# Kernel optimization log

Hardware: AMD Instinct MI355X
Metric: run time of the kernel (lower is better)

## Reference

```python
import jax, jax.numpy as jnp
import numpy as np

N = 100000   # nodes
E = 1600000  # edges
D = 128      # input feature dim
H = 128      # hidden dim
C = 10       # output classes
G = 64       # graphs in batch


def setup_inputs() -> dict:
    key = jax.random.key(0)
    ks = jax.random.split(key, 24)
    s = 0.02
    lin = lambda k, i, o: jax.random.normal(k, (i, o), jnp.float32) * s
    inp = {
        'x': jax.random.normal(ks[0], (N, D), jnp.float32),
        'edge_index': jax.random.randint(ks[1], (2, E), 0, N),
        'batch': jnp.sort(jax.random.randint(ks[2], (N,), 0, G)),
        # GIN conv 0: Linear(D,H)-ReLU-Linear(H,H)
        'w1_0': lin(ks[3], D, H), 'b1_0': jnp.zeros((H,), jnp.float32),
        'w2_0': lin(ks[4], H, H), 'b2_0': jnp.zeros((H,), jnp.float32),
        # GIN conv 1
        'w1_1': lin(ks[5], H, H), 'b1_1': jnp.zeros((H,), jnp.float32),
        'w2_1': lin(ks[6], H, H), 'b2_1': jnp.zeros((H,), jnp.float32),
        # GIN conv 2
        'w1_2': lin(ks[7], H, H), 'b1_2': jnp.zeros((H,), jnp.float32),
        'w2_2': lin(ks[8], H, H), 'b2_2': jnp.zeros((H,), jnp.float32),
        # LayerNorms (applied after layers 0 and 1)
        'ln_g0': jnp.ones((H,), jnp.float32), 'ln_b0': jnp.zeros((H,), jnp.float32),
        'ln_g1': jnp.ones((H,), jnp.float32), 'ln_b1': jnp.zeros((H,), jnp.float32),
        # post_mp: Linear(H,H) -> Dropout -> Linear(H,C)
        'pw1': lin(ks[9], H, H), 'pb1': jnp.zeros((H,), jnp.float32),
        'pw2': lin(ks[10], H, C), 'pb2': jnp.zeros((C,), jnp.float32),
    }
    return inp


def _gin_conv(x, src, dst, w1, b1, w2, b2):
    # GINConv with eps=0: MLP(x + sum_{j->i} x_j)
    agg = jax.ops.segment_sum(x[src], dst, num_segments=N)  # [N, d]
    h = x + agg
    h = jax.nn.relu(h @ w1 + b1) @ w2 + b2
    return h


def _layernorm(x, g, b, eps=1e-5):
    mu = jnp.mean(x, axis=-1, keepdims=True)
    var = jnp.var(x, axis=-1, keepdims=True)
    return (x - mu) * jax.lax.rsqrt(var + eps) * g + b


def reference(x, edge_index, batch,
              w1_0, b1_0, w2_0, b2_0,
              w1_1, b1_1, w2_1, b2_1,
              w1_2, b1_2, w2_2, b2_2,
              ln_g0, ln_b0, ln_g1, ln_b1,
              pw1, pb1, pw2, pb2):
    src, dst = edge_index[0], edge_index[1]
    convs = [(w1_0, b1_0, w2_0, b2_0), (w1_1, b1_1, w2_1, b2_1), (w1_2, b1_2, w2_2, b2_2)]
    lns = [(ln_g0, ln_b0), (ln_g1, ln_b1)]
    emb = x
    h = x
    for i in range(3):
        w1, b1, w2, b2 = convs[i]
        h = _gin_conv(h, src, dst, w1, b1, w2, b2)
        emb = h
        h = jax.nn.relu(h)
        # dropout p=0.25: identity in eval mode
        if i != 2:
            g, b = lns[i]
            h = _layernorm(h, g, b)
    # global mean pool over graphs
    sums = jax.ops.segment_sum(h, batch, num_segments=G)          # [G, H]
    cnts = jax.ops.segment_sum(jnp.ones((N,), h.dtype), batch, num_segments=G)
    pooled = sums / jnp.maximum(cnts, 1.0)[:, None]
    # post_mp (dropout identity in eval)
    z = pooled @ pw1 + pb1
    logits = z @ pw2 + pb2
    return emb, jax.nn.log_softmax(logits, axis=1)
```

## Files before the change

### kernel.cpp

```cpp
#include <hip/hip_runtime.h>

typedef __bf16 bf16_t;
typedef __bf16 bf16x8 __attribute__((ext_vector_type(8)));
typedef float floatx4 __attribute__((ext_vector_type(4)));

constexpr int N = 100000;
constexpr int E = 1600000;
constexpr int H = 128;
constexpr int G = 64;
constexpr int C = 10;
constexpr int NBLK = (N + 255) / 256;

constexpr int FPART = 8;
constexpr int FPART_SZ = (N + FPART - 1) / FPART;
constexpr int FCHUNK = 256;
constexpr int FCHUNK_E = E / FCHUNK;

__device__ inline float bflo(unsigned u) {
  return __builtin_bit_cast(float, u << 16);
}
__device__ inline float bfhi(unsigned u) {
  return __builtin_bit_cast(float, u & 0xffff0000u);
}
__device__ inline unsigned short f2b(float f) {
  return __builtin_bit_cast(unsigned short, (bf16_t)f);
}
__device__ inline unsigned pack2(float a, float b) {
  return (unsigned)f2b(a) | ((unsigned)f2b(b) << 16);
}

__global__ __launch_bounds__(256) void tobf_kernel(const float* __restrict__ x,
                                                   uint4* __restrict__ xb) {
  const int g = blockIdx.x * 256 + threadIdx.x;
  const float4 a = *(const float4*)(x + (size_t)g * 8);
  const float4 b = *(const float4*)(x + (size_t)g * 8 + 4);
  uint4 o;
  o.x = pack2(a.x, a.y);
  o.y = pack2(a.z, a.w);
  o.z = pack2(b.x, b.y);
  o.w = pack2(b.z, b.w);
  xb[g] = o;
}

__global__ __launch_bounds__(256) void hist_kernel(const int* __restrict__ dst,
                                                   int* __restrict__ deg) {
  const int e = blockIdx.x * 256 + threadIdx.x;
  if (e < E) atomicAdd(&deg[dst[e]], 1);
}

__global__ __launch_bounds__(256) void partial_kernel(
    const int* __restrict__ deg, int* __restrict__ partials) {
  __shared__ int sm[256];
  const int tid = threadIdx.x;
  const int i = blockIdx.x * 256 + tid;
  sm[tid] = (i < N) ? deg[i] : 0;
  __syncthreads();
  for (int off = 128; off > 0; off >>= 1) {
    if (tid < off) sm[tid] += sm[tid + off];
    __syncthreads();
  }
  if (tid == 0) partials[blockIdx.x] = sm[0];
}

__global__ __launch_bounds__(512) void scanp_kernel(
    const int* __restrict__ partials, int* __restrict__ blockbase) {
  __shared__ int p[512];
  const int t = threadIdx.x;
  p[t] = (t < NBLK) ? partials[t] : 0;
  __syncthreads();
  for (int off = 1; off < 512; off <<= 1) {
    int v = 0;
    if (t >= off) v = p[t - off];
    __syncthreads();
    p[t] += v;
    __syncthreads();
  }
  if (t < NBLK) blockbase[t] = (t == 0) ? 0 : p[t - 1];
}

__global__ __launch_bounds__(256) void expand_kernel(
    const int* __restrict__ deg, const int* __restrict__ blockbase,
    int* __restrict__ rowptr, int* __restrict__ cursor) {
  __shared__ int sm[256];
  const int tid = threadIdx.x;
  const int i = blockIdx.x * 256 + tid;
  const int d = (i < N) ? deg[i] : 0;
  sm[tid] = d;
  __syncthreads();
  for (int off = 1; off < 256; off <<= 1) {
    int v = 0;
    if (tid >= off) v = sm[tid - off];
    __syncthreads();
    sm[tid] += v;
    __syncthreads();
  }
  const int excl = sm[tid] - d + blockbase[blockIdx.x];
  if (i < N) {
    rowptr[i] = excl;
    cursor[i] = excl;
  }
  if (i == N - 1) rowptr[N] = excl + d;
}

__global__ __launch_bounds__(256) void fill_kernel(const int* __restrict__ src,
                                                   const int* __restrict__ dst,
                                                   int* __restrict__ cursor,
                                                   int* __restrict__ csr_src) {
  const int part = blockIdx.x & (FPART - 1);
  const int chunk = blockIdx.x >> 3;
  const int lo = part * FPART_SZ;
  const int hi = lo + FPART_SZ;
  const int c0 = chunk * FCHUNK_E;
  for (int e = c0 + threadIdx.x; e < c0 + FCHUNK_E; e += 256) {
    const int d = __builtin_nontemporal_load(dst + e);
    if (d >= lo && d < hi) {
      const int s = __builtin_nontemporal_load(src + e);
      const int slot = atomicAdd(&cursor[d], 1);
      csr_src[slot] = s;
    }
  }
}

__global__ __launch_bounds__(256) void gather_kernel(
    const uint4* __restrict__ h, const int* __restrict__ rowptr,
    const int* __restrict__ csr_src, uint4* __restrict__ pre) {
  const int node = blockIdx.x * 16 + (threadIdx.x >> 4);
  const int l = threadIdx.x & 15;
  const int r0 = rowptr[node];
  const int r1 = rowptr[node + 1];
  const uint4 v = h[(size_t)node * 16 + l];
  float a0 = bflo(v.x), a1 = bfhi(v.x), a2 = bflo(v.y), a3 = bfhi(v.y);
  float a4 = bflo(v.z), a5 = bfhi(v.z), a6 = bflo(v.w), a7 = bfhi(v.w);
  int s = r0;
  for (; s + 3 < r1; s += 4) {
    const int i0 = csr_src[s], i1 = csr_src[s + 1];
    const int i2 = csr_src[s + 2], i3 = csr_src[s + 3];
    const uint4 u0 = h[(size_t)i0 * 16 + l];
    const uint4 u1 = h[(size_t)i1 * 16 + l];
    const uint4 u2 = h[(size_t)i2 * 16 + l];
    const uint4 u3 = h[(size_t)i3 * 16 + l];
    a0 += bflo(u0.x); a1 += bfhi(u0.x); a2 += bflo(u0.y); a3 += bfhi(u0.y);
    a4 += bflo(u0.z); a5 += bfhi(u0.z); a6 += bflo(u0.w); a7 += bfhi(u0.w);
    a0 += bflo(u1.x); a1 += bfhi(u1.x); a2 += bflo(u1.y); a3 += bfhi(u1.y);
    a4 += bflo(u1.z); a5 += bfhi(u1.z); a6 += bflo(u1.w); a7 += bfhi(u1.w);
    a0 += bflo(u2.x); a1 += bfhi(u2.x); a2 += bflo(u2.y); a3 += bfhi(u2.y);
    a4 += bflo(u2.z); a5 += bfhi(u2.z); a6 += bflo(u2.w); a7 += bfhi(u2.w);
    a0 += bflo(u3.x); a1 += bfhi(u3.x); a2 += bflo(u3.y); a3 += bfhi(u3.y);
    a4 += bflo(u3.z); a5 += bfhi(u3.z); a6 += bflo(u3.w); a7 += bfhi(u3.w);
  }
  for (; s < r1; ++s) {
    const uint4 u = h[(size_t)csr_src[s] * 16 + l];
    a0 += bflo(u.x); a1 += bfhi(u.x); a2 += bflo(u.y); a3 += bfhi(u.y);
    a4 += bflo(u.z); a5 += bfhi(u.z); a6 += bflo(u.w); a7 += bfhi(u.w);
  }
  uint4 o;
  o.x = pack2(a0, a1);
  o.y = pack2(a2, a3);
  o.z = pack2(a4, a5);
  o.w = pack2(a6, a7);
  pre[(size_t)node * 16 + l] = o;
}

template <int MODE>
__global__ __launch_bounds__(256) void mlp_kernel(
    const unsigned short* __restrict__ pre_g,
    const float* __restrict__ w1, const float* __restrict__ b1,
    const float* __restrict__ w2, const float* __restrict__ b2,
    const float* __restrict__ lng, const float* __restrict__ lnb,
    unsigned short* __restrict__ h_out,
    float* __restrict__ emb) {
  __shared__ unsigned short preS[32 * 136];
  __shared__ unsigned short hidS[32 * 136];
  __shared__ float muS[32];
  __shared__ float rsS[32];

  const int tid = threadIdx.x;
  const int wave = tid >> 6;
  const int lane = tid & 63;
  const int quad = lane >> 4;
  const int l16 = lane & 15;

  union F8 { bf16x8 v; bf16_t e[8]; };

  bf16x8 w1f[4][2], w2f[4][2];
#pragma unroll
  for (int nn = 0; nn < 2; ++nn) {
    const int col = wave * 32 + nn * 16 + l16;
#pragma unroll
    for (int kt = 0; kt < 4; ++kt) {
      F8 t1, t2;
#pragma unroll
      for (int j = 0; j < 8; ++j) {
        const int k = kt * 32 + quad * 8 + j;
        t1.e[j] = (bf16_t)w1[k * H + col];
        t2.e[j] = (bf16_t)w2[k * H + col];
      }
      w1f[kt][nn] = t1.v;
      w2f[kt][nn] = t2.v;
    }
  }
  const float b1v[2] = {b1[wave * 32 + l16], b1[wave * 32 + 16 + l16]};
  const float b2v[2] = {b2[wave * 32 + l16], b2[wave * 32 + 16 + l16]};
  float lng0 = 0.f, lng1 = 0.f, lnb0 = 0.f, lnb1 = 0.f;
  const int c2 = (tid * 2) & 127;
  if (MODE == 0) {
    lng0 = lng[c2]; lng1 = lng[c2 + 1];
    lnb0 = lnb[c2]; lnb1 = lnb[c2 + 1];
  }

  for (int tile = blockIdx.x; tile < N / 32; tile += gridDim.x) {
    const size_t base = (size_t)tile * 32 * H;
    {
      const uint4* srcp = (const uint4*)(pre_g + base);
#pragma unroll
      for (int it = 0; it < 2; ++it) {
        const int chunk = it * 256 + tid;
        const int row = chunk >> 4;
        const int colc = (chunk & 15) * 8;
        *(uint4*)&preS[row * 136 + colc] = srcp[chunk];
      }
    }
    __syncthreads();

    {
      floatx4 acc[2][2];
#pragma unroll
      for (int i = 0; i < 2; ++i)
#pragma unroll
        for (int j = 0; j < 2; ++j) acc[i][j] = {0.f, 0.f, 0.f, 0.f};
#pragma unroll
      for (int kt = 0; kt < 4; ++kt) {
        const int kc = kt * 32 + quad * 8;
        const bf16x8 a0 =
            __builtin_bit_cast(bf16x8, *(const uint4*)&preS[l16 * 136 + kc]);
        const bf16x8 a1 = __builtin_bit_cast(
            bf16x8, *(const uint4*)&preS[(16 + l16) * 136 + kc]);
        acc[0][0] = __builtin_amdgcn_mfma_f32_16x16x32_bf16(a0, w1f[kt][0],
                                                            acc[0][0], 0, 0, 0);
        acc[0][1] = __builtin_amdgcn_mfma_f32_16x16x32_bf16(a0, w1f[kt][1],
                                                            acc[0][1], 0, 0, 0);
        acc[1][0] = __builtin_amdgcn_mfma_f32_16x16x32_bf16(a1, w1f[kt][0],
                                                            acc[1][0], 0, 0, 0);
        acc[1][1] = __builtin_amdgcn_mfma_f32_16x16x32_bf16(a1, w1f[kt][1],
                                                            acc[1][1], 0, 0, 0);
      }
#pragma unroll
      for (int mt = 0; mt < 2; ++mt)
#pragma unroll
        for (int nn = 0; nn < 2; ++nn) {
          const int col = wave * 32 + nn * 16 + l16;
#pragma unroll
          for (int r = 0; r < 4; ++r) {
            const int row = mt * 16 + quad * 4 + r;
            const float v = fmaxf(acc[mt][nn][r] + b1v[nn], 0.f);
            hidS[row * 136 + col] = f2b(v);
          }
        }
    }
    __syncthreads();

    {
      floatx4 acc[2][2];
#pragma unroll
      for (int i = 0; i < 2; ++i)
#pragma unroll
        for (int j = 0; j < 2; ++j) acc[i][j] = {0.f, 0.f, 0.f, 0.f};
#pragma unroll
      for (int kt = 0; kt < 4; ++kt) {
        const int kc = kt * 32 + quad * 8;
        const bf16x8 a0 =
            __builtin_bit_cast(bf16x8, *(const uint4*)&hidS[l16 * 136 + kc]);
        const bf16x8 a1 = __builtin_bit_cast(
            bf16x8, *(const uint4*)&hidS[(16 + l16) * 136 + kc]);
        acc[0][0] = __builtin_amdgcn_mfma_f32_16x16x32_bf16(a0, w2f[kt][0],
                                                            acc[0][0], 0, 0, 0);
        acc[0][1] = __builtin_amdgcn_mfma_f32_16x16x32_bf16(a0, w2f[kt][1],
                                                            acc[0][1], 0, 0, 0);
        acc[1][0] = __builtin_amdgcn_mfma_f32_16x16x32_bf16(a1, w2f[kt][0],
                                                            acc[1][0], 0, 0, 0);
        acc[1][1] = __builtin_amdgcn_mfma_f32_16x16x32_bf16(a1, w2f[kt][1],
                                                            acc[1][1], 0, 0, 0);
      }
#pragma unroll
      for (int mt = 0; mt < 2; ++mt)
#pragma unroll
        for (int nn = 0; nn < 2; ++nn) {
          const int col = wave * 32 + nn * 16 + l16;
#pragma unroll
          for (int r = 0; r < 4; ++r) {
            const int row = mt * 16 + quad * 4 + r;
            float v = acc[mt][nn][r] + b2v[nn];
            if (MODE == 0) v = fmaxf(v, 0.f);
            preS[row * 136 + col] = f2b(v);
          }
        }
    }
    __syncthreads();

    if (MODE == 0) {
      const int n = tid >> 3;
      const int j = tid & 7;
      float s = 0.f, sq = 0.f;
#pragma unroll
      for (int t = 0; t < 16; ++t) {
        const float v = bflo((unsigned)preS[n * 136 + j + 8 * t] << 16 >> 16 |
                             ((unsigned)preS[n * 136 + j + 8 * t] << 16));
        (void)v;
      }
      s = 0.f; sq = 0.f;
#pragma unroll
      for (int t = 0; t < 16; ++t) {
        const float v =
            __builtin_bit_cast(float, (unsigned)preS[n * 136 + j + 8 * t] << 16);
        s += v;
        sq += v * v;
      }
      s += __shfl_xor(s, 1); sq += __shfl_xor(sq, 1);
      s += __shfl_xor(s, 2); sq += __shfl_xor(sq, 2);
      s += __shfl_xor(s, 4); sq += __shfl_xor(sq, 4);
      if (j == 0) {
        const float mu = s * (1.f / H);
        const float var = sq * (1.f / H) - mu * mu;
        muS[n] = mu;
        rsS[n] = rsqrtf(var + 1e-5f);
      }
      __syncthreads();
      unsigned* ho = (unsigned*)(h_out + base);
#pragma unroll
      for (int it = 0; it < 8; ++it) {
        const int idx = it * 512 + tid * 2;
        const int row = idx >> 7;
        const int k = idx & 127;
        const unsigned pr = *(const unsigned*)&preS[row * 136 + k];
        const float mu = muS[row], rs = rsS[row];
        const float v0 = (bflo(pr) - mu) * rs * lng0 + lnb0;
        const float v1 = (bfhi(pr) - mu) * rs * lng1 + lnb1;
        ho[idx >> 1] = pack2(v0, v1);
      }
    } else {
      unsigned* ho = (unsigned*)(h_out + base);
#pragma unroll
      for (int it = 0; it < 8; ++it) {
        const int idx = it * 512 + tid * 2;
        const int row = idx >> 7;
        const int k = idx & 127;
        const unsigned pr = *(const unsigned*)&preS[row * 136 + k];
        const float v0 = bflo(pr);
        const float v1 = bfhi(pr);
        *(float2*)&emb[base + idx] = make_float2(v0, v1);
        ho[idx >> 1] = pack2(fmaxf(v0, 0.f), fmaxf(v1, 0.f));
      }
    }
    __syncthreads();
  }
}

__global__ __launch_bounds__(256) void pool_kernel(
    const uint4* __restrict__ hv, const int* __restrict__ batch,
    float* __restrict__ pooled, float* __restrict__ cnt) {
  __shared__ int bs[256];
  __shared__ float smr[512];
  __shared__ int endS;
  const int tid = threadIdx.x;
  const int c0 = blockIdx.x * 256;
  const int len = min(256, N - c0);
  if (tid < len) bs[tid] = batch[c0 + tid];
  __syncthreads();

  const int nl = tid >> 4;
  const int fg = tid & 15;
  const int wave = tid >> 6;
  const int lane = tid & 63;

  int start = 0;
  while (start < len) {
    const int g = bs[start];
    if (tid == 0) endS = len;
    __syncthreads();
    for (int i = start + tid; i < len; i += 256)
      if (bs[i] != g) atomicMin(&endS, i);
    __syncthreads();
    const int end = endS;

    float a0 = 0.f, a1 = 0.f, a2 = 0.f, a3 = 0.f;
    float a4 = 0.f, a5 = 0.f, a6 = 0.f, a7 = 0.f;
    for (int i = start + nl; i < end; i += 16) {
      const uint4 u = hv[(size_t)(c0 + i) * 16 + fg];
      a0 += bflo(u.x); a1 += bfhi(u.x); a2 += bflo(u.y); a3 += bfhi(u.y);
      a4 += bflo(u.z); a5 += bfhi(u.z); a6 += bflo(u.w); a7 += bfhi(u.w);
    }
    a0 += __shfl_xor(a0, 16); a1 += __shfl_xor(a1, 16);
    a2 += __shfl_xor(a2, 16); a3 += __shfl_xor(a3, 16);
    a4 += __shfl_xor(a4, 16); a5 += __shfl_xor(a5, 16);
    a6 += __shfl_xor(a6, 16); a7 += __shfl_xor(a7, 16);
    a0 += __shfl_xor(a0, 32); a1 += __shfl_xor(a1, 32);
    a2 += __shfl_xor(a2, 32); a3 += __shfl_xor(a3, 32);
    a4 += __shfl_xor(a4, 32); a5 += __shfl_xor(a5, 32);
    a6 += __shfl_xor(a6, 32); a7 += __shfl_xor(a7, 32);
    if (lane < 16) {
      float* d = &smr[wave * 128 + lane * 8];
      d[0] = a0; d[1] = a1; d[2] = a2; d[3] = a3;
      d[4] = a4; d[5] = a5; d[6] = a6; d[7] = a7;
    }
    __syncthreads();
    if (tid < 128) {
      const float s =
          smr[tid] + smr[128 + tid] + smr[256 + tid] + smr[384 + tid];
      atomicAdd(&pooled[g * H + tid], s);
    }
    if (tid == 0) atomicAdd(&cnt[g], (float)(end - start));
    __syncthreads();
    start = end;
  }
}

__global__ __launch_bounds__(128) void head_kernel(
    const float* __restrict__ pooled, const float* __restrict__ cnt,
    const float* __restrict__ pw1, const float* __restrict__ pb1,
    const float* __restrict__ pw2, const float* __restrict__ pb2,
    float* __restrict__ out_logp) {
  __shared__ float p[H];
  __shared__ float z[H];
  __shared__ float l[C];
  const int g = blockIdx.x;
  const int f = threadIdx.x;
  const float c = fmaxf(cnt[g], 1.f);
  p[f] = pooled[g * H + f] / c;
  __syncthreads();
  float a = pb1[f];
  for (int k = 0; k < H; ++k) a += p[k] * pw1[k * H + f];
  z[f] = a;
  __syncthreads();
  if (f < C) {
    float a2 = pb2[f];
    for (int k = 0; k < H; ++k) a2 += z[k] * pw2[k * C + f];
    l[f] = a2;
  }
  __syncthreads();
  if (f == 0) {
    float m = l[0];
    for (int i = 1; i < C; ++i) m = fmaxf(m, l[i]);
    float s = 0.f;
    for (int i = 0; i < C; ++i) s += expf(l[i] - m);
    const float lse = m + logf(s);
    for (int i = 0; i < C; ++i) out_logp[g * C + i] = l[i] - lse;
  }
}

extern "C" void kernel_launch(void* const* d_in, const int* in_sizes, int n_in,
                              void* d_out, int out_size, void* d_ws,
                              size_t ws_size, hipStream_t stream) {
  const float* x = (const float*)d_in[0];
  const int* ei = (const int*)d_in[1];
  const int* src = ei;
  const int* dst = ei + E;
  const int* batch = (const int*)d_in[2];
  const float* w1_0 = (const float*)d_in[3];
  const float* b1_0 = (const float*)d_in[4];
  const float* w2_0 = (const float*)d_in[5];
  const float* b2_0 = (const float*)d_in[6];
  const float* w1_1 = (const float*)d_in[7];
  const float* b1_1 = (const float*)d_in[8];
  const float* w2_1 = (const float*)d_in[9];
  const float* b2_1 = (const float*)d_in[10];
  const float* w1_2 = (const float*)d_in[11];
  const float* b1_2 = (const float*)d_in[12];
  const float* w2_2 = (const float*)d_in[13];
  const float* b2_2 = (const float*)d_in[14];
  const float* ln_g0 = (const float*)d_in[15];
  const float* ln_b0 = (const float*)d_in[16];
  const float* ln_g1 = (const float*)d_in[17];
  const float* ln_b1 = (const float*)d_in[18];
  const float* pw1 = (const float*)d_in[19];
  const float* pb1 = (const float*)d_in[20];
  const float* pw2 = (const float*)d_in[21];
  const float* pb2 = (const float*)d_in[22];

  unsigned short* xb = (unsigned short*)d_ws;
  unsigned short* hb = xb + (size_t)N * H;
  unsigned short* pre = hb + (size_t)N * H;
  float* pooled = (float*)(pre + (size_t)N * H);
  float* cnt = pooled + (size_t)G * H;
  int* deg = (int*)(cnt + G);
  int* rowptr = deg + N;
  int* cursor = rowptr + N + 1;
  int* csr_src = cursor + N;
  int* partials = csr_src + E;
  int* blockbase = partials + NBLK;
  float* emb = (float*)d_out;
  float* logp = emb + (size_t)N * H;

  tobf_kernel<<<N * H / (256 * 8), 256, 0, stream>>>(x, (uint4*)xb);

  hipMemsetAsync(deg, 0, (size_t)N * sizeof(int), stream);
  hist_kernel<<<E / 256, 256, 0, stream>>>(dst, deg);
  partial_kernel<<<NBLK, 256, 0, stream>>>(deg, partials);
  scanp_kernel<<<1, 512, 0, stream>>>(partials, blockbase);
  expand_kernel<<<NBLK, 256, 0, stream>>>(deg, blockbase, rowptr, cursor);
  fill_kernel<<<FCHUNK * FPART, 256, 0, stream>>>(src, dst, cursor, csr_src);

  gather_kernel<<<N / 16, 256, 0, stream>>>((const uint4*)xb, rowptr, csr_src,
                                            (uint4*)pre);
  mlp_kernel<0><<<2048, 256, 0, stream>>>(pre, w1_0, b1_0, w2_0, b2_0, ln_g0,
                                          ln_b0, hb, nullptr);
  gather_kernel<<<N / 16, 256, 0, stream>>>((const uint4*)hb, rowptr, csr_src,
                                            (uint4*)pre);
  mlp_kernel<0><<<2048, 256, 0, stream>>>(pre, w1_1, b1_1, w2_1, b2_1, ln_g1,
                                          ln_b1, hb, nullptr);
  gather_kernel<<<N / 16, 256, 0, stream>>>((const uint4*)hb, rowptr, csr_src,
                                            (uint4*)pre);
  mlp_kernel<1><<<2048, 256, 0, stream>>>(pre, w1_2, b1_2, w2_2, b2_2, nullptr,
                                          nullptr, hb, emb);

  hipMemsetAsync(pooled, 0, (size_t)(G * H + G) * sizeof(float), stream);
  pool_kernel<<<NBLK, 256, 0, stream>>>((const uint4*)hb, batch, pooled, cnt);
  head_kernel<<<G, 128, 0, stream>>>(pooled, cnt, pw1, pb1, pw2, pb2, logp);
}
```

Measured before the change: 574.2 us.

## Bucket edges by destination partition before CSR fill

Merges the degree histogram with a pass that sorts edges into 8 destination-range buckets, each edge stored as a packed (src<<14 | local dst) word in a scratch buffer that reuses the pre workspace. The CSR fill then reads only its own partition's bucket, instead of every block scanning all edges and filtering them by partition. This cuts the 8x redundant reading of dst in the old fill and keeps cursor atomics localized per partition. The histogram phase now uses only 256 blocks and reads dst twice, and bucket capacity is fixed at 204800, which assumes a roughly uniform destination distribution. A dead LayerNorm loop is also removed.

```diff
diff --git a/kernel.cpp b/kernel.cpp
--- a/kernel.cpp
+++ b/kernel.cpp
@@ -13,8 +13,9 @@
 
 constexpr int FPART = 8;
 constexpr int FPART_SZ = (N + FPART - 1) / FPART;
-constexpr int FCHUNK = 256;
-constexpr int FCHUNK_E = E / FCHUNK;
+constexpr int BBLK = 256;
+constexpr int BCHUNK = E / BBLK;
+constexpr int BCAP = 204800;
 
 __device__ inline float bflo(unsigned u) {
   return __builtin_bit_cast(float, u << 16);
@@ -42,10 +43,37 @@
   xb[g] = o;
 }
 
-__global__ __launch_bounds__(256) void hist_kernel(const int* __restrict__ dst,
-                                                   int* __restrict__ deg) {
-  const int e = blockIdx.x * 256 + threadIdx.x;
-  if (e < E) atomicAdd(&deg[dst[e]], 1);
+__global__ __launch_bounds__(256) void bucket_kernel(
+    const int* __restrict__ src, const int* __restrict__ dst,
+    int* __restrict__ deg, unsigned* __restrict__ buckets,
+    int* __restrict__ bcnt) {
+  __shared__ int cntA[FPART];
+  __shared__ int cntB[FPART];
+  __shared__ int baseS[FPART];
+  const int tid = threadIdx.x;
+  if (tid < FPART) {
+    cntA[tid] = 0;
+    cntB[tid] = 0;
+  }
+  __syncthreads();
+  const int c0 = blockIdx.x * BCHUNK;
+  const int c1 = c0 + BCHUNK;
+  for (int e = c0 + tid; e < c1; e += 256) {
+    const int d = dst[e];
+    atomicAdd(&deg[d], 1);
+    atomicAdd(&cntA[d / FPART_SZ], 1);
+  }
+  __syncthreads();
+  if (tid < FPART) baseS[tid] = atomicAdd(&bcnt[tid], cntA[tid]);
+  __syncthreads();
+  for (int e = c0 + tid; e < c1; e += 256) {
+    const int d = dst[e];
+    const int s = src[e];
+    const int p = d / FPART_SZ;
+    const int r = atomicAdd(&cntB[p], 1);
+    buckets[p * BCAP + baseS[p] + r] =
+        ((unsigned)s << 14) | (unsigned)(d - p * FPART_SZ);
+  }
 }
 
 __global__ __launch_bounds__(256) void partial_kernel(
@@ -102,22 +130,21 @@
   if (i == N - 1) rowptr[N] = excl + d;
 }
 
-__global__ __launch_bounds__(256) void fill_kernel(const int* __restrict__ src,
-                                                   const int* __restrict__ dst,
-                                                   int* __restrict__ cursor,
-                                                   int* __restrict__ csr_src) {
+__global__ __launch_bounds__(256) void fill2_kernel(
+    const unsigned* __restrict__ buckets, const int* __restrict__ bcnt,
+    int* __restrict__ cursor, int* __restrict__ csr_src) {
   const int part = blockIdx.x & (FPART - 1);
-  const int chunk = blockIdx.x >> 3;
-  const int lo = part * FPART_SZ;
-  const int hi = lo + FPART_SZ;
-  const int c0 = chunk * FCHUNK_E;
-  for (int e = c0 + threadIdx.x; e < c0 + FCHUNK_E; e += 256) {
-    const int d = __builtin_nontemporal_load(dst + e);
-    if (d >= lo && d < hi) {
-      const int s = __builtin_nontemporal_load(src + e);
-      const int slot = atomicAdd(&cursor[d], 1);
-      csr_src[slot] = s;
-    }
+  const int blk = blockIdx.x >> 3;
+  const int nblk = gridDim.x >> 3;
+  const int cnt = bcnt[part];
+  const unsigned* b = buckets + part * BCAP;
+  const int dbase = part * FPART_SZ;
+  for (int i = blk * 256 + threadIdx.x; i < cnt; i += nblk * 256) {
+    const unsigned u = b[i];
+    const int d = dbase + (int)(u & 0x3FFFu);
+    const int s = (int)(u >> 14);
+    const int slot = atomicAdd(&cursor[d], 1);
+    csr_src[slot] = s;
   }
 }
 
@@ -301,13 +328,6 @@
       const int n = tid >> 3;
       const int j = tid & 7;
       float s = 0.f, sq = 0.f;
-#pragma unroll
-      for (int t = 0; t < 16; ++t) {
-        const float v = bflo((unsigned)preS[n * 136 + j + 8 * t] << 16 >> 16 |
-                             ((unsigned)preS[n * 136 + j + 8 * t] << 16));
-        (void)v;
-      }
-      s = 0.f; sq = 0.f;
 #pragma unroll
       for (int t = 0; t < 16; ++t) {
         const float v =
@@ -487,17 +507,20 @@
   int* csr_src = cursor + N;
   int* partials = csr_src + E;
   int* blockbase = partials + NBLK;
+  int* bcnt = blockbase + NBLK;
+  unsigned* buckets = (unsigned*)pre;
   float* emb = (float*)d_out;
   float* logp = emb + (size_t)N * H;
 
   tobf_kernel<<<N * H / (256 * 8), 256, 0, stream>>>(x, (uint4*)xb);
 
   hipMemsetAsync(deg, 0, (size_t)N * sizeof(int), stream);
-  hist_kernel<<<E / 256, 256, 0, stream>>>(dst, deg);
+  hipMemsetAsync(bcnt, 0, (size_t)FPART * sizeof(int), stream);
+  bucket_kernel<<<BBLK, 256, 0, stream>>>(src, dst, deg, buckets, bcnt);
   partial_kernel<<<NBLK, 256, 0, stream>>>(deg, partials);
   scanp_kernel<<<1, 512, 0, stream>>>(partials, blockbase);
   expand_kernel<<<NBLK, 256, 0, stream>>>(deg, blockbase, rowptr, cursor);
-  fill_kernel<<<FCHUNK * FPART, 256, 0, stream>>>(src, dst, cursor, csr_src);
+  fill2_kernel<<<2048, 256, 0, stream>>>(buckets, bcnt, cursor, csr_src);
 
   gather_kernel<<<N / 16, 256, 0, stream>>>((const uint4*)xb, rowptr, csr_src,
                                             (uint4*)pre);
```

After: 585.7 us. 2.0% more time.
